# Kernel tuning notes

Hardware: AMD Instinct MI355X
Metric: run time of the kernel (lower is better)

## Reference

```python
import jax, jax.numpy as jnp
import numpy as np

HEAD = 16
EMB = 1024
D_K = EMB // HEAD


def setup_inputs() -> dict:
    key = jax.random.key(0)
    ks = jax.random.split(key, 11)
    B, S, E = 2, 2048, EMB
    scale = 1.0 / np.sqrt(E)
    inp = {
        "query": jax.random.normal(ks[0], (B, S, E), jnp.float32),
        "key": jax.random.normal(ks[1], (B, S, E), jnp.float32),
        "value": jax.random.normal(ks[2], (B, S, E), jnp.float32),
        "Wq": jax.random.normal(ks[3], (E, E), jnp.float32) * scale,
        "bq": jnp.zeros((E,), jnp.float32),
        "Wk": jax.random.normal(ks[4], (E, E), jnp.float32) * scale,
        "bk": jnp.zeros((E,), jnp.float32),
        "Wv": jax.random.normal(ks[5], (E, E), jnp.float32) * scale,
        "bv": jnp.zeros((E,), jnp.float32),
        "Wo": jax.random.normal(ks[6], (E, E), jnp.float32) * scale,
        "bo": jnp.zeros((E,), jnp.float32),
    }
    return inp


def reference(query, key, value, Wq, bq, Wk, bk, Wv, bv, Wo, bo):
    B, S, E = query.shape
    # 3 input projections, split into heads: [B, H, S, d_k]
    def proj(x, W, b):
        return (x @ W.T + b).reshape(B, S, HEAD, D_K).transpose(0, 2, 1, 3)

    q = proj(query, Wq, bq)
    k = proj(key, Wk, bk)
    v = proj(value, Wv, bv)

    # scaled dot-product attention (full matrix, as in original)
    scores = jnp.einsum("bhqd,bhkd->bhqk", q, k) / jnp.sqrt(jnp.float32(D_K))
    attn = jax.nn.softmax(scores, axis=-1)  # dropout in eval mode = identity
    x = jnp.einsum("bhqk,bhkd->bhqd", attn, v)

    # merge heads and output projection
    x = x.transpose(0, 2, 1, 3).reshape(B, S, E)
    return x @ Wo.T + bo
```

## Files before the change

### kernel.cpp

```cpp
#include <hip/hip_runtime.h>
#include <hip/hip_bf16.h>
#include <math.h>


constexpr int Sn = 2048;
constexpr int En = 1024;
constexpr int Hn = 16;
constexpr int Dk = 64;
constexpr int Kn = 1024;
constexpr size_t WSZ = 1048576;
constexpr size_t TSZ = 4194304;

#define QSCALE 0.18033688011112042f

typedef __bf16 bf16x8 __attribute__((ext_vector_type(8)));
typedef float  f32x4  __attribute__((ext_vector_type(4)));
typedef float  f32x16 __attribute__((ext_vector_type(16)));

union U16 { uint4 u; bf16x8 v; __hip_bfloat16 h[8]; };
union U8  { uint2 u; __hip_bfloat162 h2[2]; __hip_bfloat16 h[4]; };
union U4  { unsigned u; __hip_bfloat162 h2; };

__device__ inline U16 cvt8f(const float* __restrict__ p) {
    float4 a = *(const float4*)p;
    float4 b = *(const float4*)(p + 4);
    U16 r;
    r.h[0] = __float2bfloat16(a.x); r.h[1] = __float2bfloat16(a.y);
    r.h[2] = __float2bfloat16(a.z); r.h[3] = __float2bfloat16(a.w);
    r.h[4] = __float2bfloat16(b.x); r.h[5] = __float2bfloat16(b.y);
    r.h[6] = __float2bfloat16(b.z); r.h[7] = __float2bfloat16(b.w);
    return r;
}

__device__ inline void gload16(const __hip_bfloat16* g, __hip_bfloat16* l) {
    __builtin_amdgcn_global_load_lds(
        (const __attribute__((address_space(1))) void*)g,
        (__attribute__((address_space(3))) void*)l, 16, 0, 0);
}

template<int ROWS, int NW>
__device__ inline void stage_tile(const __hip_bfloat16* __restrict__ src, int ld,
                                  __hip_bfloat16* lds, int w, int lane) {
    int l8 = lane >> 3;
    int g = (lane & 7) ^ (l8 & 7);
    #pragma unroll
    for (int j = 0; j < ROWS / (8 * NW); ++j) {
        int c = j * NW + w;
        gload16(src + (size_t)(c * 8 + l8) * ld + g * 8, lds + c * 512);
    }
}

__global__ __launch_bounds__(256)
void cvt_w(const float* __restrict__ w0, const float* __restrict__ w1,
           const float* __restrict__ w2, const float* __restrict__ w3,
           __hip_bfloat16* __restrict__ dst)
{
    int y = blockIdx.y;
    const float* src = (y == 0) ? w0 : (y == 1) ? w1 : (y == 2) ? w2 : w3;
    size_t i = ((size_t)blockIdx.x * 256 + threadIdx.x) * 8;
    U16 r = cvt8f(src + i);
    *(uint4*)&dst[(size_t)y * WSZ + i] = r.u;
}

__global__ __launch_bounds__(256)
void cvt_x3(const float* __restrict__ q, const float* __restrict__ k,
            const float* __restrict__ v, __hip_bfloat16* __restrict__ dst)
{
    int z = blockIdx.y;
    const float* src = (z == 0) ? q : (z == 1) ? k : v;
    size_t i = ((size_t)blockIdx.x * 256 + threadIdx.x) * 8;
    U16 r = cvt8f(src + i);
    *(uint4*)&dst[(size_t)z * TSZ + i] = r.u;
}

template<int MT, int NT>
__device__ inline void gemm_core(const __hip_bfloat16* __restrict__ Ab,
                                 const __hip_bfloat16* __restrict__ Wb,
                                 __hip_bfloat16* As, __hip_bfloat16* Bs,
                                 f32x4 (&acc)[MT][NT], int w, int lane)
{
    const int l15 = lane & 15, lg = lane >> 4, l7 = lane & 7;
    const int wm = (w & 1) * (MT * 16), wn = (w >> 1) * (NT * 16);
    const int coff0 = (lg ^ l7) * 8;
    const int coff1 = ((4 + lg) ^ l7) * 8;

    #pragma unroll
    for (int i = 0; i < MT; ++i)
        #pragma unroll
        for (int j = 0; j < NT; ++j) acc[i][j] = {0.f, 0.f, 0.f, 0.f};

    for (int k0 = 0; k0 < Kn; k0 += 64) {
        stage_tile<MT * 32, 4>(Ab + k0, Kn, As, w, lane);
        stage_tile<NT * 32, 4>(Wb + k0, Kn, Bs, w, lane);
        __syncthreads();

        U16 af[MT][2], bf[NT][2];
        #pragma unroll
        for (int mt = 0; mt < MT; ++mt) {
            int r = (wm + mt * 16 + l15) * 64;
            af[mt][0].u = *(const uint4*)&As[r + coff0];
            af[mt][1].u = *(const uint4*)&As[r + coff1];
        }
        #pragma unroll
        for (int nt = 0; nt < NT; ++nt) {
            int r = (wn + nt * 16 + l15) * 64;
            bf[nt][0].u = *(const uint4*)&Bs[r + coff0];
            bf[nt][1].u = *(const uint4*)&Bs[r + coff1];
        }
        #pragma unroll
        for (int mt = 0; mt < MT; ++mt)
            #pragma unroll
            for (int nt = 0; nt < NT; ++nt) {
                acc[mt][nt] = __builtin_amdgcn_mfma_f32_16x16x32_bf16(af[mt][0].v, bf[nt][0].v, acc[mt][nt], 0, 0, 0);
                acc[mt][nt] = __builtin_amdgcn_mfma_f32_16x16x32_bf16(af[mt][1].v, bf[nt][1].v, acc[mt][nt], 0, 0, 0);
            }
        __syncthreads();
    }
}

__global__ __launch_bounds__(256)
void gemm_qkv(const __hip_bfloat16* __restrict__ X, const __hip_bfloat16* __restrict__ Wall,
              const float* __restrict__ bq, const float* __restrict__ bk,
              const float* __restrict__ bv, __hip_bfloat16* __restrict__ outbase)
{
    __shared__ __align__(16) __hip_bfloat16 As[128 * 64];
    __shared__ __align__(16) __hip_bfloat16 Bs[128 * 64];

    const int tid = threadIdx.x, w = tid >> 6, lane = tid & 63;
    const int z = blockIdx.z;
    const int blockM = blockIdx.x * 128, blockN = blockIdx.y * 128;

    f32x4 acc[4][4];
    gemm_core<4, 4>(X + (size_t)z * TSZ + (size_t)blockM * Kn,
                    Wall + (size_t)z * WSZ + (size_t)blockN * Kn,
                    As, Bs, acc, w, lane);

    const float scale = (z == 0) ? QSCALE : 1.0f;
    const float* bias = (z == 0) ? bq : (z == 1) ? bk : bv;
    __hip_bfloat16* out = outbase + (size_t)z * TSZ;

    const int l15 = lane & 15, lg = lane >> 4;
    const int wm = (w & 1) * 64, wn = (w >> 1) * 64;

    #pragma unroll
    for (int nt = 0; nt < 4; ++nt) {
        int n = blockN + wn + nt * 16 + l15;
        float bvn = bias[n] * scale;
        int h_ = n >> 6, d_ = n & 63;
        #pragma unroll
        for (int mt = 0; mt < 4; ++mt) {
            int m0 = blockM + wm + mt * 16 + lg * 4;
            int b_ = m0 >> 11, s_ = m0 & (Sn - 1);
            if (z < 2) {
                #pragma unroll
                for (int i = 0; i < 4; ++i)
                    out[(((size_t)b_ * Hn + h_) * Sn + s_ + i) * Dk + d_] =
                        __float2bfloat16(fmaf(acc[mt][nt][i], scale, bvn));
            } else {
                U8 pk;
                #pragma unroll
                for (int i = 0; i < 4; ++i)
                    pk.h[i] = __float2bfloat16(fmaf(acc[mt][nt][i], scale, bvn));
                *(uint2*)&out[(((size_t)b_ * Hn + h_) * Dk + d_) * Sn + s_] = pk.u;
            }
        }
    }
}

__global__ __launch_bounds__(256)
void gemm_out(const __hip_bfloat16* __restrict__ A, const __hip_bfloat16* __restrict__ W,
              const float* __restrict__ bias, float* __restrict__ out)
{
    __shared__ __align__(16) __hip_bfloat16 As[128 * 64];
    __shared__ __align__(16) __hip_bfloat16 Bs[64 * 64];

    const int tid = threadIdx.x, w = tid >> 6, lane = tid & 63;
    const int blockM = blockIdx.x * 128, blockN = blockIdx.y * 64;

    f32x4 acc[4][2];
    gemm_core<4, 2>(A + (size_t)blockM * Kn, W + (size_t)blockN * Kn,
                    As, Bs, acc, w, lane);

    const int l15 = lane & 15, lg = lane >> 4;
    const int wm = (w & 1) * 64, wn = (w >> 1) * 32;

    #pragma unroll
    for (int nt = 0; nt < 2; ++nt) {
        int n = blockN + wn + nt * 16 + l15;
        float bvn = bias[n];
        #pragma unroll
        for (int mt = 0; mt < 4; ++mt) {
            int m0 = blockM + wm + mt * 16 + lg * 4;
            #pragma unroll
            for (int i = 0; i < 4; ++i)
                out[(size_t)(m0 + i) * Kn + n] = acc[mt][nt][i] + bvn;
        }
    }
}

__global__ __launch_bounds__(256)
void attn(const __hip_bfloat16* __restrict__ Q, const __hip_bfloat16* __restrict__ K,
          const __hip_bfloat16* __restrict__ Vt, __hip_bfloat16* __restrict__ X)
{
    __shared__ __align__(16) __hip_bfloat16 Ks[2][64 * 64];
    __shared__ __align__(16) __hip_bfloat16 Vts[2][64 * 64];

    const int bh = blockIdx.y, q0 = blockIdx.x * 128;
    const int tid = threadIdx.x, w = tid >> 6, lane = tid & 63;
    const int l31 = lane & 31, hi = lane >> 5;

    const __hip_bfloat16* Qb = Q  + (size_t)bh * Sn * Dk;
    const __hip_bfloat16* Kb = K  + (size_t)bh * Sn * Dk;
    const __hip_bfloat16* Vb = Vt + (size_t)bh * Dk * Sn;

    U16 qf[4];
    {
        const __hip_bfloat16* qp = Qb + (size_t)(q0 + w * 32 + l31) * Dk + hi * 8;
        #pragma unroll
        for (int d0t = 0; d0t < 4; ++d0t)
            qf[d0t].u = *(const uint4*)(qp + d0t * 16);
    }

    f32x16 o[2];
    #pragma unroll
    for (int dt = 0; dt < 2; ++dt)
        #pragma unroll
        for (int r = 0; r < 16; ++r) o[dt][r] = 0.f;
    float lpart = 0.f;

    stage_tile<64, 4>(Kb, Dk, Ks[0], w, lane);
    stage_tile<64, 4>(Vb, Sn, Vts[0], w, lane);

    for (int t = 0; t < Sn / 64; ++t) {
        __syncthreads();
        const int cur = t & 1;
        if (t + 1 < Sn / 64) {
            stage_tile<64, 4>(Kb + (size_t)(t + 1) * 64 * Dk, Dk, Ks[cur ^ 1], w, lane);
            stage_tile<64, 4>(Vb + (t + 1) * 64, Sn, Vts[cur ^ 1], w, lane);
        }

        f32x16 st[2];
        #pragma unroll
        for (int kt = 0; kt < 2; ++kt)
            #pragma unroll
            for (int r = 0; r < 16; ++r) st[kt][r] = 0.f;

        #pragma unroll
        for (int d0t = 0; d0t < 4; ++d0t) {
            #pragma unroll
            for (int kt = 0; kt < 2; ++kt) {
                int r = kt * 32 + l31;
                int col = (((d0t * 2 + hi)) ^ (r & 7)) * 8;
                U16 kf; kf.u = *(const uint4*)&Ks[cur][r * 64 + col];
                st[kt] = __builtin_amdgcn_mfma_f32_32x32x16_bf16(kf.v, qf[d0t].v, st[kt], 0, 0, 0);
            }
        }

        uint4 pa[4];
        #pragma unroll
        for (int kt = 0; kt < 2; ++kt) {
            float pv[16];
            #pragma unroll
            for (int r = 0; r < 16; ++r) pv[r] = __builtin_amdgcn_exp2f(st[kt][r]);
            float s01 = (pv[0] + pv[1]) + (pv[2] + pv[3]);
            float s23 = (pv[4] + pv[5]) + (pv[6] + pv[7]);
            float s45 = (pv[8] + pv[9]) + (pv[10] + pv[11]);
            float s67 = (pv[12] + pv[13]) + (pv[14] + pv[15]);
            lpart += (s01 + s23) + (s45 + s67);

            uint wv[8];
            #pragma unroll
            for (int m2 = 0; m2 < 8; ++m2) {
                U4 pk; pk.h2 = __float22bfloat162_rn({pv[2 * m2], pv[2 * m2 + 1]});
                wv[m2] = pk.u;
            }
            asm volatile("v_permlane32_swap_b32 %0, %1" : "+v"(wv[0]), "+v"(wv[2]));
            asm volatile("v_permlane32_swap_b32 %0, %1" : "+v"(wv[1]), "+v"(wv[3]));
            asm volatile("v_permlane32_swap_b32 %0, %1" : "+v"(wv[4]), "+v"(wv[6]));
            asm volatile("v_permlane32_swap_b32 %0, %1" : "+v"(wv[5]), "+v"(wv[7]));
            pa[kt * 2 + 0] = make_uint4(wv[0], wv[1], wv[2], wv[3]);
            pa[kt * 2 + 1] = make_uint4(wv[4], wv[5], wv[6], wv[7]);
        }

        #pragma unroll
        for (int k0t = 0; k0t < 4; ++k0t) {
            U16 pau; pau.u = pa[k0t];
            #pragma unroll
            for (int dt = 0; dt < 2; ++dt) {
                int r = dt * 32 + l31;
                int col = (((k0t * 2 + hi)) ^ (r & 7)) * 8;
                U16 vf; vf.u = *(const uint4*)&Vts[cur][r * 64 + col];
                o[dt] = __builtin_amdgcn_mfma_f32_32x32x16_bf16(pau.v, vf.v, o[dt], 0, 0, 0);
            }
        }
    }

    lpart += __shfl_xor(lpart, 32, 64);
    float linv = 1.f / lpart;

    float li[16];
    #pragma unroll
    for (int r = 0; r < 16; ++r) {
        int qr = (r & 3) + 8 * (r >> 2) + 4 * hi;
        li[r] = __shfl(linv, qr, 64);
    }

    int b_ = bh >> 4, h_ = bh & (Hn - 1);
    #pragma unroll
    for (int r = 0; r < 16; ++r) {
        int qr = (r & 3) + 8 * (r >> 2) + 4 * hi;
        int sr = q0 + w * 32 + qr;
        __hip_bfloat16* xp = X + ((size_t)(b_ * Sn + sr)) * En + h_ * Dk + l31;
        xp[0]  = __float2bfloat16(o[0][r] * li[r]);
        xp[32] = __float2bfloat16(o[1][r] * li[r]);
    }
}

extern "C" void kernel_launch(void* const* d_in, const int* in_sizes, int n_in,
                              void* d_out, int out_size, void* d_ws, size_t ws_size,
                              hipStream_t stream)
{
    const float* query = (const float*)d_in[0];
    const float* key   = (const float*)d_in[1];
    const float* value = (const float*)d_in[2];
    const float* Wq = (const float*)d_in[3];
    const float* bq = (const float*)d_in[4];
    const float* Wk = (const float*)d_in[5];
    const float* bk = (const float*)d_in[6];
    const float* Wv = (const float*)d_in[7];
    const float* bv = (const float*)d_in[8];
    const float* Wo = (const float*)d_in[9];
    const float* bo = (const float*)d_in[10];
    float* out = (float*)d_out;

    __hip_bfloat16* xqkv = (__hip_bfloat16*)d_ws;
    __hip_bfloat16* Wbf  = xqkv + 3 * TSZ;
    __hip_bfloat16* QKVw = Wbf + 4 * WSZ;
    __hip_bfloat16* Xw   = xqkv;

    cvt_w<<<dim3(512, 4), 256, 0, stream>>>(Wq, Wk, Wv, Wo, Wbf);
    cvt_x3<<<dim3(2048, 3), 256, 0, stream>>>(query, key, value, xqkv);
    gemm_qkv<<<dim3(32, 8, 3), 256, 0, stream>>>(xqkv, Wbf, bq, bk, bv, QKVw);
    attn<<<dim3(Sn / 128, 32), 256, 0, stream>>>(QKVw, QKVw + TSZ, QKVw + 2 * TSZ, Xw);
    gemm_out<<<dim3(32, 16), 256, 0, stream>>>(Xw, Wbf + 3 * WSZ, bo, out);
}
```

Baseline: 231.1 us.

## Deepen attention K/V prefetch to four stages and halve GEMM M tiles

```diff
diff --git a/kernel.cpp b/kernel.cpp
--- a/kernel.cpp
+++ b/kernel.cpp
@@ -73,30 +73,30 @@
     *(uint4*)&dst[(size_t)z * TSZ + i] = r.u;
 }
 
-template<int MT, int NT>
+template<int NT>
 __device__ inline void gemm_core(const __hip_bfloat16* __restrict__ Ab,
                                  const __hip_bfloat16* __restrict__ Wb,
                                  __hip_bfloat16* As, __hip_bfloat16* Bs,
-                                 f32x4 (&acc)[MT][NT], int w, int lane)
+                                 f32x4 (&acc)[2][NT], int w, int lane)
 {
     const int l15 = lane & 15, lg = lane >> 4, l7 = lane & 7;
-    const int wm = (w & 1) * (MT * 16), wn = (w >> 1) * (NT * 16);
+    const int wm = (w & 1) * 32, wn = (w >> 1) * (NT * 16);
     const int coff0 = (lg ^ l7) * 8;
     const int coff1 = ((4 + lg) ^ l7) * 8;
 
     #pragma unroll
-    for (int i = 0; i < MT; ++i)
+    for (int i = 0; i < 2; ++i)
         #pragma unroll
         for (int j = 0; j < NT; ++j) acc[i][j] = {0.f, 0.f, 0.f, 0.f};
 
     for (int k0 = 0; k0 < Kn; k0 += 64) {
-        stage_tile<MT * 32, 4>(Ab + k0, Kn, As, w, lane);
+        stage_tile<64, 4>(Ab + k0, Kn, As, w, lane);
         stage_tile<NT * 32, 4>(Wb + k0, Kn, Bs, w, lane);
         __syncthreads();
 
-        U16 af[MT][2], bf[NT][2];
-        #pragma unroll
-        for (int mt = 0; mt < MT; ++mt) {
+        U16 af[2][2], bf[NT][2];
+        #pragma unroll
+        for (int mt = 0; mt < 2; ++mt) {
             int r = (wm + mt * 16 + l15) * 64;
             af[mt][0].u = *(const uint4*)&As[r + coff0];
             af[mt][1].u = *(const uint4*)&As[r + coff1];
@@ -108,7 +108,7 @@
             bf[nt][1].u = *(const uint4*)&Bs[r + coff1];
         }
         #pragma unroll
-        for (int mt = 0; mt < MT; ++mt)
+        for (int mt = 0; mt < 2; ++mt)
             #pragma unroll
             for (int nt = 0; nt < NT; ++nt) {
                 acc[mt][nt] = __builtin_amdgcn_mfma_f32_16x16x32_bf16(af[mt][0].v, bf[nt][0].v, acc[mt][nt], 0, 0, 0);
@@ -123,24 +123,24 @@
               const float* __restrict__ bq, const float* __restrict__ bk,
               const float* __restrict__ bv, __hip_bfloat16* __restrict__ outbase)
 {
-    __shared__ __align__(16) __hip_bfloat16 As[128 * 64];
+    __shared__ __align__(16) __hip_bfloat16 As[64 * 64];
     __shared__ __align__(16) __hip_bfloat16 Bs[128 * 64];
 
     const int tid = threadIdx.x, w = tid >> 6, lane = tid & 63;
     const int z = blockIdx.z;
-    const int blockM = blockIdx.x * 128, blockN = blockIdx.y * 128;
-
-    f32x4 acc[4][4];
-    gemm_core<4, 4>(X + (size_t)z * TSZ + (size_t)blockM * Kn,
-                    Wall + (size_t)z * WSZ + (size_t)blockN * Kn,
-                    As, Bs, acc, w, lane);
+    const int blockM = blockIdx.x * 64, blockN = blockIdx.y * 128;
+
+    f32x4 acc[2][4];
+    gemm_core<4>(X + (size_t)z * TSZ + (size_t)blockM * Kn,
+                 Wall + (size_t)z * WSZ + (size_t)blockN * Kn,
+                 As, Bs, acc, w, lane);
 
     const float scale = (z == 0) ? QSCALE : 1.0f;
     const float* bias = (z == 0) ? bq : (z == 1) ? bk : bv;
     __hip_bfloat16* out = outbase + (size_t)z * TSZ;
 
     const int l15 = lane & 15, lg = lane >> 4;
-    const int wm = (w & 1) * 64, wn = (w >> 1) * 64;
+    const int wm = (w & 1) * 32, wn = (w >> 1) * 64;
 
     #pragma unroll
     for (int nt = 0; nt < 4; ++nt) {
@@ -148,7 +148,7 @@
         float bvn = bias[n] * scale;
         int h_ = n >> 6, d_ = n & 63;
         #pragma unroll
-        for (int mt = 0; mt < 4; ++mt) {
+        for (int mt = 0; mt < 2; ++mt) {
             int m0 = blockM + wm + mt * 16 + lg * 4;
             int b_ = m0 >> 11, s_ = m0 & (Sn - 1);
             if (z < 2) {
@@ -171,25 +171,25 @@
 void gemm_out(const __hip_bfloat16* __restrict__ A, const __hip_bfloat16* __restrict__ W,
               const float* __restrict__ bias, float* __restrict__ out)
 {
-    __shared__ __align__(16) __hip_bfloat16 As[128 * 64];
+    __shared__ __align__(16) __hip_bfloat16 As[64 * 64];
     __shared__ __align__(16) __hip_bfloat16 Bs[64 * 64];
 
     const int tid = threadIdx.x, w = tid >> 6, lane = tid & 63;
-    const int blockM = blockIdx.x * 128, blockN = blockIdx.y * 64;
-
-    f32x4 acc[4][2];
-    gemm_core<4, 2>(A + (size_t)blockM * Kn, W + (size_t)blockN * Kn,
-                    As, Bs, acc, w, lane);
+    const int blockM = blockIdx.x * 64, blockN = blockIdx.y * 64;
+
+    f32x4 acc[2][2];
+    gemm_core<2>(A + (size_t)blockM * Kn, W + (size_t)blockN * Kn,
+                 As, Bs, acc, w, lane);
 
     const int l15 = lane & 15, lg = lane >> 4;
-    const int wm = (w & 1) * 64, wn = (w >> 1) * 32;
+    const int wm = (w & 1) * 32, wn = (w >> 1) * 32;
 
     #pragma unroll
     for (int nt = 0; nt < 2; ++nt) {
         int n = blockN + wn + nt * 16 + l15;
         float bvn = bias[n];
         #pragma unroll
-        for (int mt = 0; mt < 4; ++mt) {
+        for (int mt = 0; mt < 2; ++mt) {
             int m0 = blockM + wm + mt * 16 + lg * 4;
             #pragma unroll
             for (int i = 0; i < 4; ++i)
@@ -202,8 +202,8 @@
 void attn(const __hip_bfloat16* __restrict__ Q, const __hip_bfloat16* __restrict__ K,
           const __hip_bfloat16* __restrict__ Vt, __hip_bfloat16* __restrict__ X)
 {
-    __shared__ __align__(16) __hip_bfloat16 Ks[2][64 * 64];
-    __shared__ __align__(16) __hip_bfloat16 Vts[2][64 * 64];
+    __shared__ __align__(16) __hip_bfloat16 Ks[4][64 * 64];
+    __shared__ __align__(16) __hip_bfloat16 Vts[4][64 * 64];
 
     const int bh = blockIdx.y, q0 = blockIdx.x * 128;
     const int tid = threadIdx.x, w = tid >> 6, lane = tid & 63;
@@ -220,6 +220,7 @@
         for (int d0t = 0; d0t < 4; ++d0t)
             qf[d0t].u = *(const uint4*)(qp + d0t * 16);
     }
+    asm volatile("s_waitcnt vmcnt(0)" ::: "memory");
 
     f32x16 o[2];
     #pragma unroll
@@ -228,16 +229,23 @@
         for (int r = 0; r < 16; ++r) o[dt][r] = 0.f;
     float lpart = 0.f;
 
-    stage_tile<64, 4>(Kb, Dk, Ks[0], w, lane);
-    stage_tile<64, 4>(Vb, Sn, Vts[0], w, lane);
+    #pragma unroll
+    for (int p = 0; p < 3; ++p) {
+        stage_tile<64, 4>(Kb + (size_t)p * 64 * Dk, Dk, Ks[p], w, lane);
+        stage_tile<64, 4>(Vb + p * 64, Sn, Vts[p], w, lane);
+    }
 
     for (int t = 0; t < Sn / 64; ++t) {
-        __syncthreads();
-        const int cur = t & 1;
-        if (t + 1 < Sn / 64) {
-            stage_tile<64, 4>(Kb + (size_t)(t + 1) * 64 * Dk, Dk, Ks[cur ^ 1], w, lane);
-            stage_tile<64, 4>(Vb + (t + 1) * 64, Sn, Vts[cur ^ 1], w, lane);
-        }
+        asm volatile("s_waitcnt vmcnt(8)" ::: "memory");
+        __builtin_amdgcn_s_barrier();
+        __builtin_amdgcn_sched_barrier(0);
+
+        const int ts = (t + 3) & 31;
+        const int sb = (t + 3) & 3;
+        stage_tile<64, 4>(Kb + (size_t)ts * 64 * Dk, Dk, Ks[sb], w, lane);
+        stage_tile<64, 4>(Vb + ts * 64, Sn, Vts[sb], w, lane);
+
+        const int cur = t & 3;
 
         f32x16 st[2];
         #pragma unroll
@@ -245,6 +253,7 @@
             #pragma unroll
             for (int r = 0; r < 16; ++r) st[kt][r] = 0.f;
 
+        __builtin_amdgcn_s_setprio(1);
         #pragma unroll
         for (int d0t = 0; d0t < 4; ++d0t) {
             #pragma unroll
@@ -255,6 +264,7 @@
                 st[kt] = __builtin_amdgcn_mfma_f32_32x32x16_bf16(kf.v, qf[d0t].v, st[kt], 0, 0, 0);
             }
         }
+        __builtin_amdgcn_s_setprio(0);
 
         uint4 pa[4];
         #pragma unroll
@@ -282,6 +292,7 @@
             pa[kt * 2 + 1] = make_uint4(wv[4], wv[5], wv[6], wv[7]);
         }
 
+        __builtin_amdgcn_s_setprio(1);
         #pragma unroll
         for (int k0t = 0; k0t < 4; ++k0t) {
             U16 pau; pau.u = pa[k0t];
@@ -293,7 +304,10 @@
                 o[dt] = __builtin_amdgcn_mfma_f32_32x32x16_bf16(pau.v, vf.v, o[dt], 0, 0, 0);
             }
         }
-    }
+        __builtin_amdgcn_s_setprio(0);
+    }
+
+    asm volatile("s_waitcnt vmcnt(0)" ::: "memory");
 
     lpart += __shfl_xor(lpart, 32, 64);
     float linv = 1.f / lpart;
@@ -340,7 +354,7 @@
 
     cvt_w<<<dim3(512, 4), 256, 0, stream>>>(Wq, Wk, Wv, Wo, Wbf);
     cvt_x3<<<dim3(2048, 3), 256, 0, stream>>>(query, key, value, xqkv);
-    gemm_qkv<<<dim3(32, 8, 3), 256, 0, stream>>>(xqkv, Wbf, bq, bk, bv, QKVw);
+    gemm_qkv<<<dim3(64, 8, 3), 256, 0, stream>>>(xqkv, Wbf, bq, bk, bv, QKVw);
     attn<<<dim3(Sn / 128, 32), 256, 0, stream>>>(QKVw, QKVw + TSZ, QKVw + 2 * TSZ, Xw);
-    gemm_out<<<dim3(32, 16), 256, 0, stream>>>(Xw, Wbf + 3 * WSZ, bo, out);
-}
+    gemm_out<<<dim3(64, 16), 256, 0, stream>>>(Xw, Wbf + 3 * WSZ, bo, out);
+}
```

Measured after the change: 237.9 us. +2.9%, slower.
